# Kernel optimization log

Measured on AMD Instinct MI355X. Metric: run time of the kernel, lower is better.

## Reference

```python
import jax, jax.numpy as jnp
import numpy as np

PIXELS_PER_CELL = (8, 8)
CELLS_PER_BLOCK = (2, 2)
ORIENTATIONS = 9
GRAY_W = jnp.array([0.2125, 0.7154, 0.0721], dtype=jnp.float32)  # skimage rgb2gray
EPS = 1e-5  # skimage L2-Hys eps


def setup_inputs() -> dict:
    key = jax.random.key(0)
    x = jax.random.uniform(key, (64, 512, 512, 3), dtype=jnp.float32)
    return {"x": x}


def _hog(x):
    # rgb2gray
    gray = jnp.einsum("bhwc,c->bhw", x, GRAY_W)  # [B,H,W]
    B, H, W = gray.shape
    pr, pc = PIXELS_PER_CELL
    br, bc = CELLS_PER_BLOCK
    O = ORIENTATIONS

    # skimage _hog_channel_gradient: central differences, zero at borders
    g_row = jnp.zeros_like(gray).at[:, 1:-1, :].set(gray[:, 2:, :] - gray[:, :-2, :])
    g_col = jnp.zeros_like(gray).at[:, :, 1:-1].set(gray[:, :, 2:] - gray[:, :, :-2])

    mag = jnp.hypot(g_row, g_col)
    ori = jnp.rad2deg(jnp.arctan2(g_row, g_col)) % 180.0  # unsigned orientation

    ncr, ncc = H // pr, W // pc
    mag = mag[:, : ncr * pr, : ncc * pc]
    ori = ori[:, : ncr * pr, : ncc * pc]

    spacing = 180.0 / O
    cell_area = float(pr * pc)
    # per-orientation-bin cell histograms: hard binning (skimage cell_hog)
    hists = []
    for o in range(O):
        lo, hi = spacing * o, spacing * (o + 1)
        contrib = jnp.where((ori >= lo) & (ori < hi), mag, 0.0)
        # sum over each pr x pc cell, divide by cell area
        h = contrib.reshape(B, ncr, pr, ncc, pc).sum(axis=(2, 4)) / cell_area
        hists.append(h)
    hist = jnp.stack(hists, axis=-1)  # [B, ncr, ncc, O]

    # overlapping blocks of cells, stride 1 cell
    nbr, nbc = ncr - br + 1, ncc - bc + 1
    block = jnp.stack(
        [jnp.stack([hist[:, r : r + nbr, c : c + nbc, :] for c in range(bc)], axis=3)
         for r in range(br)], axis=3)  # [B, nbr, nbc, br, bc, O]

    # L2-Hys normalization (skimage default block_norm)
    norm = jnp.sqrt(jnp.sum(block * block, axis=(3, 4, 5), keepdims=True) + EPS ** 2)
    blk = jnp.minimum(block / norm, 0.2)
    norm2 = jnp.sqrt(jnp.sum(blk * blk, axis=(3, 4, 5), keepdims=True) + EPS ** 2)
    blk = blk / norm2

    return blk.reshape(B, -1).astype(jnp.float32)


def reference(x):
    return _hog(x)
```

## Files before the change

### kernel.cpp

```cpp
#include <hip/hip_runtime.h>
#include <math.h>

#define IMG_H 512
#define IMG_W 512
#define NCELL 64
#define NORI 9

__device__ __noinline__ float fdlibm_atanf(float x) {
#pragma clang fp contract(off)
    const float atanhi[4] = {4.6364760399e-01f, 7.8539812565e-01f,
                             9.8279368877e-01f, 1.5707962513e+00f};
    const float atanlo[4] = {5.0121582440e-09f, 3.7748947079e-08f,
                             3.4473217170e-08f, 7.5497894159e-08f};
    const float aT[11] = {
        3.3333334327e-01f, -2.0000000298e-01f, 1.4285714924e-01f,
       -1.1111110449e-01f,  9.0908870101e-02f, -7.6918758452e-02f,
        6.6610731184e-02f, -5.8335702866e-02f,  4.9768779427e-02f,
       -3.6531571299e-02f,  1.6285819933e-02f};
    const float one = 1.0f;

    int hx = __float_as_int(x);
    int ix = hx & 0x7fffffff;
    int id;
    if (ix >= 0x4c800000) {
        if (hx > 0) return atanhi[3] + atanlo[3];
        else        return -atanhi[3] - atanlo[3];
    }
    if (ix < 0x3ee00000) {
        if (ix < 0x39800000) {
            return x;
        }
        id = -1;
    } else {
        x = fabsf(x);
        if (ix < 0x3f980000) {
            if (ix < 0x3f300000) { id = 0; x = (2.0f * x - one) / (2.0f + x); }
            else                 { id = 1; x = (x - one) / (x + one); }
        } else {
            if (ix < 0x401c0000) { id = 2; x = (x - 1.5f) / (one + 1.5f * x); }
            else                 { id = 3; x = -1.0f / x; }
        }
    }
    float z = x * x;
    float w = z * z;
    float s1 = z * (aT[0] + w * (aT[2] + w * (aT[4] + w * (aT[6] + w * (aT[8] + w * aT[10])))));
    float s2 = w * (aT[1] + w * (aT[3] + w * (aT[5] + w * (aT[7] + w * aT[9]))));
    if (id < 0) return x - x * (s1 + s2);
    z = atanhi[id] - ((x * (s1 + s2) - atanlo[id]) - x);
    return (hx < 0) ? -z : z;
}

__device__ __noinline__ int fdlibm_bin(float y, float x) {
#pragma clang fp contract(off)
    const float tiny   = 1.0e-30f;
    const float pi_o_2 = 1.5707963705e+00f;
    const float pi     = 3.1415927410e+00f;
    const float pi_lo  = -8.7422776573e-08f;

    int hx = __float_as_int(x), ix = hx & 0x7fffffff;
    int hy = __float_as_int(y), iy = hy & 0x7fffffff;
    float th;
    if (hx == 0x3f800000) { th = fdlibm_atanf(y); }
    else {
        int m = ((hy >> 31) & 1) | ((hx >> 30) & 2);
        if (iy == 0) {
            switch (m) {
                case 0:
                case 1: th = y; break;
                case 2: th =  pi + tiny; break;
                default: th = -pi - tiny; break;
            }
        } else if (ix == 0) {
            th = (hy < 0) ? -pi_o_2 - tiny : pi_o_2 + tiny;
        } else {
            int k = (iy - ix) >> 23;
            float z;
            int mm = m;
            if (k > 26) {
                z = pi_o_2 + 0.5f * pi_lo;
                mm &= 1;
            } else if (k < -26 && hx < 0) {
                z = 0.0f;
            } else {
                z = fdlibm_atanf(fabsf(y / x));
            }
            switch (mm) {
                case 0:  th = z; break;
                case 1:  th = -z; break;
                case 2:  th = pi - (z - pi_lo); break;
                default: th = (z - pi_lo) - pi; break;
            }
        }
    }
    const float RAD2DEG = (float)(180.0 / 3.14159265358979311600e+00);
    float m = fmodf(th * RAD2DEG, 180.0f);
    if (m < 0.0f) m += 180.0f;
    int o = (int)(m * 0.05f);
    if (o < 9) {
        if (m < 20.0f * (float)o) --o;
        else if (m >= 20.0f * (float)(o + 1)) ++o;
    }
    return o;
}

__global__ __launch_bounds__(256) void hog_hist_kernel(const float* __restrict__ x,
                                                       float* __restrict__ hist) {
#pragma clang fp contract(off)
    const int bid = blockIdx.x;
    const int b   = bid >> 6;
    const int cr  = bid & 63;
    const int t   = threadIdx.x;
    const int h0  = cr * 8;

    __shared__ __align__(16) float g[10][IMG_W];
    __shared__ float cellHist[NCELL * NORI];

    for (int i = t; i < NCELL * NORI; i += 256) cellHist[i] = 0.0f;

    const float GW0 = 0.2125f, GW1 = 0.7154f, GW2 = 0.0721f;
    for (int gi = t; gi < 10 * 128; gi += 256) {
        const int rr = gi >> 7;
        int h = h0 - 1 + rr;
        if (h < 0)      h = 1;
        if (h > 511)    h = 510;
        const int grp = gi & 127;
        const float4* p4 = (const float4*)x + (size_t)(b * IMG_H + h) * (IMG_W * 3 / 4)
                           + (size_t)grp * 3;
        float4 a = p4[0], c = p4[1], d = p4[2];
        const int wg = grp * 4;
        g[rr][wg + 0] = __builtin_fmaf(a.z, GW2, __builtin_fmaf(a.y, GW1, a.x * GW0));
        g[rr][wg + 1] = __builtin_fmaf(c.y, GW2, __builtin_fmaf(c.x, GW1, a.w * GW0));
        g[rr][wg + 2] = __builtin_fmaf(d.x, GW2, __builtin_fmaf(c.w, GW1, c.z * GW0));
        g[rr][wg + 3] = __builtin_fmaf(d.w, GW2, __builtin_fmaf(d.z, GW1, d.y * GW0));
    }
    __syncthreads();

    const float PIF   = 3.14159265358979323846f;
    const float PIO2F = 1.57079632679489662f;
    const float PIO4F = 0.78539816339744831f;
    for (int pass = 0; pass < 2; ++pass) {
        const int w  = t + pass * 256;
        const int wl = (w == 0)   ? 0   : w - 1;
        const int wr = (w == 511) ? 511 : w + 1;
        const bool wok = (w >= 1) && (w <= 510);
        const int cellBase = (w >> 3) * NORI;

        float cc[10], ee[8], ww[8];
#pragma unroll
        for (int i = 0; i < 10; ++i) cc[i] = g[i][w];
#pragma unroll
        for (int i = 0; i < 8; ++i) { ee[i] = g[i + 1][wr]; ww[i] = g[i + 1][wl]; }

#pragma unroll
        for (int r = 0; r < 8; ++r) {
            const float gr = cc[r + 2] - cc[r];
            const float gc = wok ? (ee[r] - ww[r]) : 0.0f;
            const float mag = __builtin_amdgcn_sqrtf(__builtin_fmaf(gr, gr, gc * gc));

            const float ax = fabsf(gc), ay = fabsf(gr);
            const float mx = fmaxf(ax, ay), mn = fminf(ax, ay);
            const bool red = mn > 0.4142135624f * mx;
            const float num = red ? (mn - mx) : mn;
            const float den = red ? (mn + mx) : mx;
            const float xx  = num * __builtin_amdgcn_rcpf(den);
            const float z   = xx * xx;
            float y = __builtin_fmaf(
                        __builtin_fmaf(
                          __builtin_fmaf(8.05374449538e-2f, z, -1.38776856032e-1f),
                          z, 1.99777106478e-1f),
                        z, -3.33329491539e-1f);
            float r0 = __builtin_fmaf(y * z, xx, xx);
            if (red)        r0 = PIO4F + r0;
            if (ay > ax)    r0 = PIO2F - r0;
            if (gc < 0.0f)  r0 = PIF - r0;
            if (gr < 0.0f)  r0 = PIF - r0;
            const float q    = (r0 * 57.295779513082323f) * 0.05f;
            int o            = (int)q;
            const float frac = q - (float)o;
            if (frac < 1e-4f || frac > 0.9999f || o > 8) {
                o = fdlibm_bin(gr, gc);
                if (o < 0 || o > 8) continue;
            }
            atomicAdd(&cellHist[cellBase + o], mag);
        }
    }
    __syncthreads();

    float* hout = hist + (size_t)(b * NCELL + cr) * (NCELL * NORI);
    for (int i = t; i < NCELL * NORI; i += 256) hout[i] = cellHist[i] * 0.015625f;
}

__global__ __launch_bounds__(256) void hog_norm_kernel(const float* __restrict__ hist,
                                                       float* __restrict__ out) {
#pragma clang fp contract(off)
    const int bid = blockIdx.x;
    const int b   = bid / 63;
    const int r   = bid % 63;
    const int t   = threadIdx.x;

    __shared__ __align__(16) float hrow[2 * NCELL * NORI];
    __shared__ __align__(16) float orow[63 * 36];

    const float4* src = (const float4*)(hist + (size_t)(b * NCELL + r) * (NCELL * NORI));
    float4* dst = (float4*)hrow;
    for (int i = t; i < 288; i += 256) dst[i] = src[i];
    __syncthreads();

    const int c = t >> 2;
    const int l = t & 3;
    if (c < 63) {
        const int bi = l >> 1, bj = l & 1;
        const float* v = &hrow[(bi * NCELL + (c + bj)) * NORI];
        float vv[9];
        float ss = 0.0f;
#pragma unroll
        for (int k = 0; k < 9; ++k) { vv[k] = v[k]; ss += vv[k] * vv[k]; }
        ss += __shfl_xor(ss, 1, 64);
        ss += __shfl_xor(ss, 2, 64);
        const float n1 = sqrtf(ss + 1e-10f);
        float ss2 = 0.0f;
#pragma unroll
        for (int k = 0; k < 9; ++k) { vv[k] = fminf(vv[k] / n1, 0.2f); ss2 += vv[k] * vv[k]; }
        ss2 += __shfl_xor(ss2, 1, 64);
        ss2 += __shfl_xor(ss2, 2, 64);
        const float n2 = sqrtf(ss2 + 1e-10f);
        float* od = &orow[c * 36 + l * 9];
#pragma unroll
        for (int k = 0; k < 9; ++k) od[k] = vv[k] / n2;
    }
    __syncthreads();

    float4* og = (float4*)(out + (size_t)bid * (63 * 36));
    const float4* os = (const float4*)orow;
    for (int i = t; i < 567; i += 256) og[i] = os[i];
}

extern "C" void kernel_launch(void* const* d_in, const int* in_sizes, int n_in,
                              void* d_out, int out_size, void* d_ws, size_t ws_size,
                              hipStream_t stream) {
    const float* x = (const float*)d_in[0];
    float* out     = (float*)d_out;
    float* hist    = (float*)d_ws;

    hog_hist_kernel<<<dim3(64 * 64), dim3(256), 0, stream>>>(x, hist);
    hog_norm_kernel<<<dim3(64 * 63), dim3(256), 0, stream>>>(hist, out);
}
```

Measured before the change: 336.6 us.

## Fuse histogram and block normalization into one streaming kernel with rolling gray buffer

Replaces the two-kernel pipeline with a single kernel where each 512-thread block streams 8 cell rows of one image. It keeps a 3-slot ring of gray rows in LDS and prefetches the next cell row while computing the current one. LDS atomics are replaced by per-thread register bins plus a shuffle reduction. The fallback atan routines are inlined, and block normalization runs right after two adjacent histogram rows are ready, so the intermediate histogram no longer goes through global memory. The cost is far fewer blocks (512), with two barriers per row and more register pressure, which could reduce parallelism and latency hiding.

```diff
diff --git a/kernel.cpp b/kernel.cpp
--- a/kernel.cpp
+++ b/kernel.cpp
@@ -6,30 +6,18 @@
 #define NCELL 64
 #define NORI 9
 
-__device__ __noinline__ float fdlibm_atanf(float x) {
+__device__ __forceinline__ float fdlibm_atanf_inl(float x) {
 #pragma clang fp contract(off)
-    const float atanhi[4] = {4.6364760399e-01f, 7.8539812565e-01f,
-                             9.8279368877e-01f, 1.5707962513e+00f};
-    const float atanlo[4] = {5.0121582440e-09f, 3.7748947079e-08f,
-                             3.4473217170e-08f, 7.5497894159e-08f};
-    const float aT[11] = {
-        3.3333334327e-01f, -2.0000000298e-01f, 1.4285714924e-01f,
-       -1.1111110449e-01f,  9.0908870101e-02f, -7.6918758452e-02f,
-        6.6610731184e-02f, -5.8335702866e-02f,  4.9768779427e-02f,
-       -3.6531571299e-02f,  1.6285819933e-02f};
     const float one = 1.0f;
-
     int hx = __float_as_int(x);
     int ix = hx & 0x7fffffff;
     int id;
     if (ix >= 0x4c800000) {
-        if (hx > 0) return atanhi[3] + atanlo[3];
-        else        return -atanhi[3] - atanlo[3];
+        const float v = 1.5707962513e+00f + 7.5497894159e-08f;
+        return (hx > 0) ? v : -v;
     }
     if (ix < 0x3ee00000) {
-        if (ix < 0x39800000) {
-            return x;
-        }
+        if (ix < 0x39800000) return x;
         id = -1;
     } else {
         x = fabsf(x);
@@ -43,14 +31,20 @@
     }
     float z = x * x;
     float w = z * z;
-    float s1 = z * (aT[0] + w * (aT[2] + w * (aT[4] + w * (aT[6] + w * (aT[8] + w * aT[10])))));
-    float s2 = w * (aT[1] + w * (aT[3] + w * (aT[5] + w * (aT[7] + w * aT[9]))));
+    float s1 = z * (3.3333334327e-01f + w * (1.4285714924e-01f + w * (9.0908870101e-02f
+             + w * (6.6610731184e-02f + w * (4.9768779427e-02f + w * 1.6285819933e-02f)))));
+    float s2 = w * (-2.0000000298e-01f + w * (-1.1111110449e-01f + w * (-7.6918758452e-02f
+             + w * (-5.8335702866e-02f + w * -3.6531571299e-02f))));
     if (id < 0) return x - x * (s1 + s2);
-    z = atanhi[id] - ((x * (s1 + s2) - atanlo[id]) - x);
+    const float hi = (id == 0) ? 4.6364760399e-01f : (id == 1) ? 7.8539812565e-01f
+                   : (id == 2) ? 9.8279368877e-01f : 1.5707962513e+00f;
+    const float lo = (id == 0) ? 5.0121582440e-09f : (id == 1) ? 3.7748947079e-08f
+                   : (id == 2) ? 3.4473217170e-08f : 7.5497894159e-08f;
+    z = hi - ((x * (s1 + s2) - lo) - x);
     return (hx < 0) ? -z : z;
 }
 
-__device__ __noinline__ int fdlibm_bin(float y, float x) {
+__device__ __forceinline__ int fdlibm_bin_inl(float y, float x) {
 #pragma clang fp contract(off)
     const float tiny   = 1.0e-30f;
     const float pi_o_2 = 1.5707963705e+00f;
@@ -60,7 +54,7 @@
     int hx = __float_as_int(x), ix = hx & 0x7fffffff;
     int hy = __float_as_int(y), iy = hy & 0x7fffffff;
     float th;
-    if (hx == 0x3f800000) { th = fdlibm_atanf(y); }
+    if (hx == 0x3f800000) { th = fdlibm_atanf_inl(y); }
     else {
         int m = ((hy >> 31) & 1) | ((hx >> 30) & 2);
         if (iy == 0) {
@@ -82,7 +76,7 @@
             } else if (k < -26 && hx < 0) {
                 z = 0.0f;
             } else {
-                z = fdlibm_atanf(fabsf(y / x));
+                z = fdlibm_atanf_inl(fabsf(y / x));
             }
             switch (mm) {
                 case 0:  th = z; break;
@@ -103,58 +97,98 @@
     return o;
 }
 
-__global__ __launch_bounds__(256) void hog_hist_kernel(const float* __restrict__ x,
-                                                       float* __restrict__ hist) {
+__global__ __launch_bounds__(512, 4) void hog_fused_kernel(const float* __restrict__ x,
+                                                           float* __restrict__ out) {
 #pragma clang fp contract(off)
     const int bid = blockIdx.x;
-    const int b   = bid >> 6;
-    const int cr  = bid & 63;
+    const int b   = bid >> 3;
+    const int s   = bid & 7;
+    const int r0  = s * 8;
+    const int SL  = (s == 7) ? 7 : 8;
     const int t   = threadIdx.x;
-    const int h0  = cr * 8;
-
-    __shared__ __align__(16) float g[10][IMG_W];
-    __shared__ float cellHist[NCELL * NORI];
-
-    for (int i = t; i < NCELL * NORI; i += 256) cellHist[i] = 0.0f;
+
+    __shared__ __align__(16) float gbuf[3][8][IMG_W];
+    __shared__ __align__(16) float histL[2][NCELL * NORI];
 
     const float GW0 = 0.2125f, GW1 = 0.7154f, GW2 = 0.0721f;
-    for (int gi = t; gi < 10 * 128; gi += 256) {
-        const int rr = gi >> 7;
-        int h = h0 - 1 + rr;
-        if (h < 0)      h = 1;
-        if (h > 511)    h = 510;
-        const int grp = gi & 127;
-        const float4* p4 = (const float4*)x + (size_t)(b * IMG_H + h) * (IMG_W * 3 / 4)
-                           + (size_t)grp * 3;
-        float4 a = p4[0], c = p4[1], d = p4[2];
-        const int wg = grp * 4;
-        g[rr][wg + 0] = __builtin_fmaf(a.z, GW2, __builtin_fmaf(a.y, GW1, a.x * GW0));
-        g[rr][wg + 1] = __builtin_fmaf(c.y, GW2, __builtin_fmaf(c.x, GW1, a.w * GW0));
-        g[rr][wg + 2] = __builtin_fmaf(d.x, GW2, __builtin_fmaf(c.w, GW1, c.z * GW0));
-        g[rr][wg + 3] = __builtin_fmaf(d.w, GW2, __builtin_fmaf(d.z, GW1, d.y * GW0));
-    }
-    __syncthreads();
-
     const float PIF   = 3.14159265358979323846f;
     const float PIO2F = 1.57079632679489662f;
     const float PIO4F = 0.78539816339744831f;
-    for (int pass = 0; pass < 2; ++pass) {
-        const int w  = t + pass * 256;
-        const int wl = (w == 0)   ? 0   : w - 1;
-        const int wr = (w == 511) ? 511 : w + 1;
-        const bool wok = (w >= 1) && (w <= 510);
-        const int cellBase = (w >> 3) * NORI;
-
+
+    {
+        float4 A[6], C[6], D[6];
+#pragma unroll
+        for (int k = 0; k < 6; ++k) {
+            const int gi = k >> 1;
+            const int pq = t + 512 * (k & 1);
+            const int rr = pq >> 7, grp = pq & 127;
+            int h = (r0 - 1 + gi) * 8 + rr;
+            if (h < 0)   h = 1;
+            if (h > 511) h = 510;
+            const float4* p4 = (const float4*)x + (size_t)(b * IMG_H + h) * (IMG_W * 3 / 4)
+                               + (size_t)grp * 3;
+            A[k] = p4[0]; C[k] = p4[1]; D[k] = p4[2];
+        }
+#pragma unroll
+        for (int k = 0; k < 6; ++k) {
+            const int gi = k >> 1;
+            const int sl = (r0 - 1 + gi + 3) % 3;
+            const int pq = t + 512 * (k & 1);
+            const int rr = pq >> 7, wg = (pq & 127) * 4;
+            float4 gv;
+            gv.x = __builtin_fmaf(A[k].z, GW2, __builtin_fmaf(A[k].y, GW1, A[k].x * GW0));
+            gv.y = __builtin_fmaf(C[k].y, GW2, __builtin_fmaf(C[k].x, GW1, A[k].w * GW0));
+            gv.z = __builtin_fmaf(D[k].x, GW2, __builtin_fmaf(C[k].w, GW1, C[k].z * GW0));
+            gv.w = __builtin_fmaf(D[k].w, GW2, __builtin_fmaf(D[k].z, GW1, D[k].y * GW0));
+            *(float4*)&gbuf[sl][rr][wg] = gv;
+        }
+    }
+    __syncthreads();
+
+    const int w   = t;
+    const int wl  = (w == 0)   ? 0   : w - 1;
+    const int wr  = (w == 511) ? 511 : w + 1;
+    const bool wok = (w >= 1) && (w <= 510);
+    const int c   = w >> 3;
+    const int jl  = t & 7;
+
+    for (int r = r0; r <= r0 + SL; ++r) {
+        const bool pf = (r < r0 + SL);
+        float4 A[2], C[2], D[2];
+        if (pf) {
+#pragma unroll
+            for (int k = 0; k < 2; ++k) {
+                const int pq = t + 512 * k;
+                const int rr = pq >> 7, grp = pq & 127;
+                int h = (r + 2) * 8 + rr;
+                if (h > 511) h = 510;
+                const float4* p4 = (const float4*)x + (size_t)(b * IMG_H + h) * (IMG_W * 3 / 4)
+                                   + (size_t)grp * 3;
+                A[k] = p4[0]; C[k] = p4[1]; D[k] = p4[2];
+            }
+        }
+
+        const int slA = (r + 2) % 3;
+        const int slB = r % 3;
+        const int slC = (r + 1) % 3;
         float cc[10], ee[8], ww[8];
-#pragma unroll
-        for (int i = 0; i < 10; ++i) cc[i] = g[i][w];
-#pragma unroll
-        for (int i = 0; i < 8; ++i) { ee[i] = g[i + 1][wr]; ww[i] = g[i + 1][wl]; }
-
-#pragma unroll
-        for (int r = 0; r < 8; ++r) {
-            const float gr = cc[r + 2] - cc[r];
-            const float gc = wok ? (ee[r] - ww[r]) : 0.0f;
+        cc[0] = gbuf[slA][7][w];
+        cc[9] = gbuf[slC][0][w];
+#pragma unroll
+        for (int i = 0; i < 8; ++i) {
+            cc[i + 1] = gbuf[slB][i][w];
+            ee[i]     = gbuf[slB][i][wr];
+            ww[i]     = gbuf[slB][i][wl];
+        }
+
+        float bh[9];
+#pragma unroll
+        for (int k = 0; k < 9; ++k) bh[k] = 0.0f;
+
+#pragma unroll
+        for (int j = 0; j < 8; ++j) {
+            const float gr = cc[j + 2] - cc[j];
+            const float gc = wok ? (ee[j] - ww[j]) : 0.0f;
             const float mag = __builtin_amdgcn_sqrtf(__builtin_fmaf(gr, gr, gc * gc));
 
             const float ax = fabsf(gc), ay = fabsf(gr);
@@ -169,70 +203,77 @@
                           __builtin_fmaf(8.05374449538e-2f, z, -1.38776856032e-1f),
                           z, 1.99777106478e-1f),
                         z, -3.33329491539e-1f);
-            float r0 = __builtin_fmaf(y * z, xx, xx);
-            if (red)        r0 = PIO4F + r0;
-            if (ay > ax)    r0 = PIO2F - r0;
-            if (gc < 0.0f)  r0 = PIF - r0;
-            if (gr < 0.0f)  r0 = PIF - r0;
-            const float q    = (r0 * 57.295779513082323f) * 0.05f;
+            float r0a = __builtin_fmaf(y * z, xx, xx);
+            if (red)        r0a = PIO4F + r0a;
+            if (ay > ax)    r0a = PIO2F - r0a;
+            if (gc < 0.0f)  r0a = PIF - r0a;
+            if (gr < 0.0f)  r0a = PIF - r0a;
+            const float q    = (r0a * 57.295779513082323f) * 0.05f;
             int o            = (int)q;
             const float frac = q - (float)o;
-            if (frac < 1e-4f || frac > 0.9999f || o > 8) {
-                o = fdlibm_bin(gr, gc);
-                if (o < 0 || o > 8) continue;
-            }
-            atomicAdd(&cellHist[cellBase + o], mag);
-        }
-    }
-    __syncthreads();
-
-    float* hout = hist + (size_t)(b * NCELL + cr) * (NCELL * NORI);
-    for (int i = t; i < NCELL * NORI; i += 256) hout[i] = cellHist[i] * 0.015625f;
-}
-
-__global__ __launch_bounds__(256) void hog_norm_kernel(const float* __restrict__ hist,
-                                                       float* __restrict__ out) {
-#pragma clang fp contract(off)
-    const int bid = blockIdx.x;
-    const int b   = bid / 63;
-    const int r   = bid % 63;
-    const int t   = threadIdx.x;
-
-    __shared__ __align__(16) float hrow[2 * NCELL * NORI];
-    __shared__ __align__(16) float orow[63 * 36];
-
-    const float4* src = (const float4*)(hist + (size_t)(b * NCELL + r) * (NCELL * NORI));
-    float4* dst = (float4*)hrow;
-    for (int i = t; i < 288; i += 256) dst[i] = src[i];
-    __syncthreads();
-
-    const int c = t >> 2;
-    const int l = t & 3;
-    if (c < 63) {
-        const int bi = l >> 1, bj = l & 1;
-        const float* v = &hrow[(bi * NCELL + (c + bj)) * NORI];
-        float vv[9];
-        float ss = 0.0f;
-#pragma unroll
-        for (int k = 0; k < 9; ++k) { vv[k] = v[k]; ss += vv[k] * vv[k]; }
-        ss += __shfl_xor(ss, 1, 64);
-        ss += __shfl_xor(ss, 2, 64);
-        const float n1 = sqrtf(ss + 1e-10f);
-        float ss2 = 0.0f;
-#pragma unroll
-        for (int k = 0; k < 9; ++k) { vv[k] = fminf(vv[k] / n1, 0.2f); ss2 += vv[k] * vv[k]; }
-        ss2 += __shfl_xor(ss2, 1, 64);
-        ss2 += __shfl_xor(ss2, 2, 64);
-        const float n2 = sqrtf(ss2 + 1e-10f);
-        float* od = &orow[c * 36 + l * 9];
-#pragma unroll
-        for (int k = 0; k < 9; ++k) od[k] = vv[k] / n2;
-    }
-    __syncthreads();
-
-    float4* og = (float4*)(out + (size_t)bid * (63 * 36));
-    const float4* os = (const float4*)orow;
-    for (int i = t; i < 567; i += 256) og[i] = os[i];
+            bool suspect = (frac < 1e-4f) || (frac > 0.9999f) || (o > 8);
+            if (ay == 0.0f) { o = 0; suspect = false; }
+            if (__builtin_expect(suspect, 0)) {
+                o = fdlibm_bin_inl(gr, gc);
+            }
+#pragma unroll
+            for (int k = 0; k < 9; ++k) bh[k] += (o == k) ? mag : 0.0f;
+        }
+
+#pragma unroll
+        for (int k = 0; k < 9; ++k) {
+            bh[k] += __shfl_xor(bh[k], 1, 64);
+            bh[k] += __shfl_xor(bh[k], 2, 64);
+            bh[k] += __shfl_xor(bh[k], 4, 64);
+        }
+        float mv = bh[0];
+#pragma unroll
+        for (int k = 1; k < 8; ++k) mv = (jl == k) ? bh[k] : mv;
+        histL[r & 1][c * NORI + jl] = mv * 0.015625f;
+        if (jl == 0) histL[r & 1][c * NORI + 8] = bh[8] * 0.015625f;
+
+        __syncthreads();
+
+        if (pf) {
+#pragma unroll
+            for (int k = 0; k < 2; ++k) {
+                const int pq = t + 512 * k;
+                const int rr = pq >> 7, wg = (pq & 127) * 4;
+                float4 gv;
+                gv.x = __builtin_fmaf(A[k].z, GW2, __builtin_fmaf(A[k].y, GW1, A[k].x * GW0));
+                gv.y = __builtin_fmaf(C[k].y, GW2, __builtin_fmaf(C[k].x, GW1, A[k].w * GW0));
+                gv.z = __builtin_fmaf(D[k].x, GW2, __builtin_fmaf(C[k].w, GW1, C[k].z * GW0));
+                gv.w = __builtin_fmaf(D[k].w, GW2, __builtin_fmaf(D[k].z, GW1, D[k].y * GW0));
+                *(float4*)&gbuf[slA][rr][wg] = gv;
+            }
+        }
+
+        if (r > r0 && t < 252) {
+            const int cb = t >> 2;
+            const int l  = t & 3;
+            const int bi = l >> 1, bj = l & 1;
+            const int br = r - 1;
+            const float* v = &histL[(br + bi) & 1][(cb + bj) * NORI];
+            float vv[9];
+            float ss = 0.0f;
+#pragma unroll
+            for (int k = 0; k < 9; ++k) { vv[k] = v[k]; ss += vv[k] * vv[k]; }
+            ss += __shfl_xor(ss, 1, 64);
+            ss += __shfl_xor(ss, 2, 64);
+            const float rn1 = 1.0f / sqrtf(ss + 1e-10f);
+            float ss2 = 0.0f;
+#pragma unroll
+            for (int k = 0; k < 9; ++k) { vv[k] = fminf(vv[k] * rn1, 0.2f); ss2 += vv[k] * vv[k]; }
+            ss2 += __shfl_xor(ss2, 1, 64);
+            ss2 += __shfl_xor(ss2, 2, 64);
+            const float rn2 = 1.0f / sqrtf(ss2 + 1e-10f);
+            float* od = out + (size_t)(b * 63 + br) * (63 * 36) + (cb * 36 + l * 9);
+#pragma unroll
+            for (int k = 0; k < 9; ++k) od[k] = vv[k] * rn2;
+        }
+
+        __syncthreads();
+    }
 }
 
 extern "C" void kernel_launch(void* const* d_in, const int* in_sizes, int n_in,
@@ -240,8 +281,7 @@
                               hipStream_t stream) {
     const float* x = (const float*)d_in[0];
     float* out     = (float*)d_out;
-    float* hist    = (float*)d_ws;
-
-    hog_hist_kernel<<<dim3(64 * 64), dim3(256), 0, stream>>>(x, hist);
-    hog_norm_kernel<<<dim3(64 * 63), dim3(256), 0, stream>>>(hist, out);
-}
+    (void)d_ws; (void)ws_size;
+
+    hog_fused_kernel<<<dim3(64 * 8), dim3(512), 0, stream>>>(x, out);
+}
```

New measurement: 307.8 us. 8.6% less time.
